# Kernel optimization log

Measured on AMD Instinct MI355X. Metric: run time of the kernel, lower is better.

Reference implementation:

```python
import jax, jax.numpy as jnp
import numpy as np

T, B, S = 8, 64, 32
DS, DT, F, H, L = 3136, 3136, 512, 512, 18
TAU = 2.0      # braincog default tau for LIFNode and all ThreeCompNode compartments
TH_MC = 1.0    # ThreeCompNode threshold
TH_LIF = 0.5   # LIFNode threshold


def setup_inputs() -> dict:
    key = jax.random.key(0)
    ks = jax.random.split(key, 6)
    return {
        "state_embedding": jax.random.normal(ks[0], (T, B, DS), jnp.float32),
        "tau_embedding": jax.random.normal(ks[1], (T, B * S, DT), jnp.float32),
        "Wb": jax.random.normal(ks[2], (F, DS), jnp.float32) * 0.02,  # basal_w (no bias)
        "Wa": jax.random.normal(ks[3], (F, DT), jnp.float32) * 0.02,  # apical_w (no bias)
        "W1": jax.random.normal(ks[4], (H, F), jnp.float32) * 0.02,
        "b1": jnp.zeros((H,), jnp.float32),
        "W2": jax.random.normal(ks[5], (L, H), jnp.float32) * 0.02,
        "b2": jnp.zeros((L,), jnp.float32),
    }


def _spike(x):
    # heaviside spike (surrogate gradient only matters for backward)
    return (x > 0).astype(x.dtype)


def reference(state_embedding, tau_embedding, Wb, Wa, W1, b1, W2, b2):
    def step(carry, inp):
        mb, ma, ms, ml = carry
        se, te = inp
        basal = (se @ Wb.T)[:, None, :]          # [B,1,F]
        apical = (te @ Wa.T).reshape(B, S, F)    # [B,S,F]
        # ThreeCompNode integral
        mb = mb + (basal - mb) / TAU
        ma = ma + (apical - ma) / TAU
        ms = ms + (ma + mb - ms) / TAU           # broadcasts to [B,S,F]
        sp = _spike(ms - TH_MC)
        ms = ms * (1.0 - jax.lax.stop_gradient(sp))  # hard reset (detached spike)
        # _last: Linear -> LIFNode -> Linear
        h = sp.reshape(B * S, F) @ W1.T + b1     # [B*S,H]
        ml = ml + (h - ml) / TAU
        sp2 = _spike(ml - TH_LIF)
        ml = ml * (1.0 - jax.lax.stop_gradient(sp2))
        out = sp2 @ W2.T + b2                    # [B*S,L]
        return (mb, ma, ms, ml), out

    init = (
        jnp.zeros((B, 1, F), jnp.float32),
        jnp.zeros((B, S, F), jnp.float32),
        jnp.zeros((B, S, F), jnp.float32),
        jnp.zeros((B * S, H), jnp.float32),
    )
    _, outs = jax.lax.scan(step, init, (state_embedding, tau_embedding))
    q = outs.mean(axis=0)                        # sum over time / time_window
    return jnp.swapaxes(q.reshape(B, S, L), 1, 2)  # [B, L, S]
```

## Files before the change

kernel.cpp:

```cpp
#include <hip/hip_runtime.h>

typedef _Float16 f16x8 __attribute__((ext_vector_type(8)));
typedef _Float16 f16x4 __attribute__((ext_vector_type(4)));
typedef float    f32x4 __attribute__((ext_vector_type(4)));

#define SPLIT_SCALE 4096.0f
#define SPLIT_INV   (1.0f / 4096.0f)

__device__ __forceinline__ void gld_lds16(const void* g, void* l) {
    __builtin_amdgcn_global_load_lds(
        (const __attribute__((address_space(1))) unsigned int*)g,
        (__attribute__((address_space(3))) unsigned int*)l,
        16, 0, 0);
}

__device__ __forceinline__ void cvt8(const float4 a, const float4 b,
                                     f16x8& h, f16x8& l) {
    float v[8] = {a.x, a.y, a.z, a.w, b.x, b.y, b.z, b.w};
#pragma unroll
    for (int j = 0; j < 8; ++j) {
        _Float16 x = (_Float16)v[j];
        h[j] = x;
        l[j] = (_Float16)((v[j] - (float)x) * SPLIT_SCALE);
    }
}

__global__ __launch_bounds__(256) void k_cvt(
    const float* __restrict__ src, _Float16* __restrict__ h, _Float16* __restrict__ l)
{
    const size_t i = ((size_t)blockIdx.x * 256 + threadIdx.x) * 8;
    float4 v0 = *(const float4*)(src + i);
    float4 v1 = *(const float4*)(src + i + 4);
    f16x8 hh, ll;
    cvt8(v0, v1, hh, ll);
    *(f16x8*)(h + i) = hh;
    *(f16x8*)(l + i) = ll;
}

__device__ __forceinline__ void front_core(
    const float* __restrict__ A,
    const _Float16* __restrict__ Bh_g, const _Float16* __restrict__ Bl_g,
    float* __restrict__ C, int K, int m0, int n0, int nIt)
{
    __shared__ _Float16 BhL[2][128 * 64];
    __shared__ _Float16 BlL[2][128 * 64];

    const int tid  = threadIdx.x;
    const int lane = tid & 63;
    const int wave = tid >> 6;
    const int quad = lane >> 4;
    const int l15  = lane & 15;

    const int srow   = wave * 32 + (lane >> 3);
    const int schunk = (((lane & 7) ^ ((lane >> 3) & 7))) * 8;
    const size_t gB  = (size_t)(n0 + srow) * (size_t)K + schunk;
    const int ldsw   = (wave * 32) * 64;

    const float* A0 = A + (size_t)(m0 + wave * 32 + l15) * (size_t)K + quad * 8;
    const float* A1 = A0 + (size_t)16 * K;

    f32x4 accm[2][8], accc[2][8];
#pragma unroll
    for (int i = 0; i < 2; ++i)
#pragma unroll
        for (int j = 0; j < 8; ++j) {
            accm[i][j] = (f32x4){0.f, 0.f, 0.f, 0.f};
            accc[i][j] = (f32x4){0.f, 0.f, 0.f, 0.f};
        }

    float4 ar[8];
    f16x8 fah[2][2], fal[2][2];

#pragma unroll
    for (int j = 0; j < 4; ++j) {
        gld_lds16(Bh_g + gB + (size_t)(8 * j) * K, BhL[0] + ldsw + 8 * j * 64);
        gld_lds16(Bl_g + gB + (size_t)(8 * j) * K, BlL[0] + ldsw + 8 * j * 64);
    }
    ar[0] = *(const float4*)(A0);      ar[1] = *(const float4*)(A0 + 4);
    ar[2] = *(const float4*)(A0 + 32); ar[3] = *(const float4*)(A0 + 36);
    ar[4] = *(const float4*)(A1);      ar[5] = *(const float4*)(A1 + 4);
    ar[6] = *(const float4*)(A1 + 32); ar[7] = *(const float4*)(A1 + 36);
#pragma unroll
    for (int i = 0; i < 2; ++i)
#pragma unroll
        for (int kc = 0; kc < 2; ++kc)
            cvt8(ar[i * 4 + kc * 2], ar[i * 4 + kc * 2 + 1], fah[i][kc], fal[i][kc]);

    for (int it = 0; it < nIt; ++it) {
        __syncthreads();
        const int cur = it & 1;
        const int nxt = cur ^ 1;
        const bool more = (it + 1) < nIt;

        if (more) {
            const size_t kb = (size_t)(it + 1) * 64;
#pragma unroll
            for (int j = 0; j < 4; ++j) {
                gld_lds16(Bh_g + gB + (size_t)(8 * j) * K + kb, BhL[nxt] + ldsw + 8 * j * 64);
                gld_lds16(Bl_g + gB + (size_t)(8 * j) * K + kb, BlL[nxt] + ldsw + 8 * j * 64);
            }
            const float* p0 = A0 + kb;
            const float* p1 = A1 + kb;
            ar[0] = *(const float4*)(p0);      ar[1] = *(const float4*)(p0 + 4);
            ar[2] = *(const float4*)(p0 + 32); ar[3] = *(const float4*)(p0 + 36);
            ar[4] = *(const float4*)(p1);      ar[5] = *(const float4*)(p1 + 4);
            ar[6] = *(const float4*)(p1 + 32); ar[7] = *(const float4*)(p1 + 36);
        }

#pragma unroll
        for (int kc = 0; kc < 2; ++kc) {
#pragma unroll
            for (int jh = 0; jh < 2; ++jh) {
                f16x8 fbh[4], fbl[4];
#pragma unroll
                for (int j = 0; j < 4; ++j) {
                    const int jj = jh * 4 + j;
                    const int p  = (((kc * 4 + quad) ^ (l15 & 7))) * 8;
                    const int e  = (jj * 16 + l15) * 64 + p;
                    fbh[j] = *(const f16x8*)&BhL[cur][e];
                    fbl[j] = *(const f16x8*)&BlL[cur][e];
                }
#pragma unroll
                for (int i = 0; i < 2; ++i)
#pragma unroll
                    for (int j = 0; j < 4; ++j) {
                        const int jj = jh * 4 + j;
                        accm[i][jj] = __builtin_amdgcn_mfma_f32_16x16x32_f16(fah[i][kc], fbh[j], accm[i][jj], 0, 0, 0);
                        accc[i][jj] = __builtin_amdgcn_mfma_f32_16x16x32_f16(fah[i][kc], fbl[j], accc[i][jj], 0, 0, 0);
                        accc[i][jj] = __builtin_amdgcn_mfma_f32_16x16x32_f16(fal[i][kc], fbh[j], accc[i][jj], 0, 0, 0);
                    }
            }
        }

        if (more) {
#pragma unroll
            for (int i = 0; i < 2; ++i)
#pragma unroll
                for (int kc = 0; kc < 2; ++kc)
                    cvt8(ar[i * 4 + kc * 2], ar[i * 4 + kc * 2 + 1], fah[i][kc], fal[i][kc]);
        }
    }

#pragma unroll
    for (int i = 0; i < 2; ++i)
#pragma unroll
        for (int jj = 0; jj < 8; ++jj)
#pragma unroll
            for (int r = 0; r < 4; ++r) {
                const int row = m0 + wave * 32 + i * 16 + quad * 4 + r;
                const int col = n0 + jj * 16 + l15;
                C[(size_t)row * 512 + col] = accm[i][jj][r] + accc[i][jj][r] * SPLIT_INV;
            }
}

__global__ __launch_bounds__(256, 2) void k_front(
    const float* __restrict__ TE, const float* __restrict__ SE,
    const _Float16* __restrict__ Wah, const _Float16* __restrict__ Wal,
    const _Float16* __restrict__ Wbh, const _Float16* __restrict__ Wbl,
    float* __restrict__ Abuf, float* __restrict__ PCb)
{
    const int bid = blockIdx.x;
    front_core(TE, Wah, Wal, Abuf, 3136, (bid & 127) * 128, (bid >> 7) * 128, 49);

    if (bid < 256) {
        __syncthreads();
        const int p   = bid >> 4;
        const int it0 = 3 * p;
        const int nIt = (p == 15) ? 4 : 3;
        const int m0  = (bid & 3) * 128;
        const int n0  = ((bid >> 2) & 3) * 128;
        front_core(SE + it0 * 64, Wbh + it0 * 64, Wbl + it0 * 64,
                   PCb + (size_t)p * 262144, 3136, m0, n0, nIt);
    }
}

__global__ __launch_bounds__(256) void k_comb(
    const float* __restrict__ PCb, float* __restrict__ Cb)
{
    const int i = (blockIdx.x * 256 + threadIdx.x) * 4;
    double s0 = 0.0, s1 = 0.0, s2 = 0.0, s3 = 0.0;
#pragma unroll
    for (int p = 0; p < 16; ++p) {
        float4 v = *(const float4*)(PCb + (size_t)p * 262144 + i);
        s0 += v.x; s1 += v.y; s2 += v.z; s3 += v.w;
    }
    *(float4*)(Cb + i) = make_float4((float)s0, (float)s1, (float)s2, (float)s3);
}

__global__ __launch_bounds__(256, 2) void k_gemm3(
    const _Float16* __restrict__ SPh, const _Float16* __restrict__ W1h,
    const _Float16* __restrict__ W1l, float* __restrict__ H)
{
    __shared__ _Float16 BhL[2][128 * 64];
    __shared__ _Float16 BlL[2][128 * 64];

    const int bid = blockIdx.x;
    const int m0 = (bid & 127) * 128, n0 = (bid >> 7) * 128;
    const int tid  = threadIdx.x;
    const int lane = tid & 63;
    const int wave = tid >> 6;
    const int quad = lane >> 4;
    const int l15  = lane & 15;

    const int srow   = wave * 32 + (lane >> 3);
    const int schunk = (((lane & 7) ^ ((lane >> 3) & 7))) * 8;
    const size_t gB  = (size_t)(n0 + srow) * 512 + schunk;
    const int ldsw   = (wave * 32) * 64;

    const _Float16* A0 = SPh + (size_t)(m0 + wave * 32 + l15) * 512 + quad * 8;
    const _Float16* A1 = A0 + (size_t)16 * 512;

    f32x4 accm[2][8], accl[2][8];
#pragma unroll
    for (int i = 0; i < 2; ++i)
#pragma unroll
        for (int j = 0; j < 8; ++j) {
            accm[i][j] = (f32x4){0.f, 0.f, 0.f, 0.f};
            accl[i][j] = (f32x4){0.f, 0.f, 0.f, 0.f};
        }

#pragma unroll
    for (int j = 0; j < 4; ++j) {
        gld_lds16(W1h + gB + (size_t)(8 * j) * 512, BhL[0] + ldsw + 8 * j * 64);
        gld_lds16(W1l + gB + (size_t)(8 * j) * 512, BlL[0] + ldsw + 8 * j * 64);
    }

    for (int it = 0; it < 8; ++it) {
        __syncthreads();
        const int cur = it & 1;
        const int nxt = cur ^ 1;
        if (it + 1 < 8) {
            const size_t kb = (size_t)(it + 1) * 64;
#pragma unroll
            for (int j = 0; j < 4; ++j) {
                gld_lds16(W1h + gB + (size_t)(8 * j) * 512 + kb, BhL[nxt] + ldsw + 8 * j * 64);
                gld_lds16(W1l + gB + (size_t)(8 * j) * 512 + kb, BlL[nxt] + ldsw + 8 * j * 64);
            }
        }
        f16x8 fa[2][2];
        const size_t ka = (size_t)it * 64;
#pragma unroll
        for (int i = 0; i < 2; ++i)
#pragma unroll
            for (int kc = 0; kc < 2; ++kc)
                fa[i][kc] = *(const f16x8*)((i ? A1 : A0) + ka + kc * 32);

#pragma unroll
        for (int kc = 0; kc < 2; ++kc) {
#pragma unroll
            for (int jh = 0; jh < 2; ++jh) {
                f16x8 fbh[4], fbl[4];
#pragma unroll
                for (int j = 0; j < 4; ++j) {
                    const int jj = jh * 4 + j;
                    const int p  = (((kc * 4 + quad) ^ (l15 & 7))) * 8;
                    const int e  = (jj * 16 + l15) * 64 + p;
                    fbh[j] = *(const f16x8*)&BhL[cur][e];
                    fbl[j] = *(const f16x8*)&BlL[cur][e];
                }
#pragma unroll
                for (int i = 0; i < 2; ++i)
#pragma unroll
                    for (int j = 0; j < 4; ++j) {
                        const int jj = jh * 4 + j;
                        accm[i][jj] = __builtin_amdgcn_mfma_f32_16x16x32_f16(fa[i][kc], fbh[j], accm[i][jj], 0, 0, 0);
                        accl[i][jj] = __builtin_amdgcn_mfma_f32_16x16x32_f16(fa[i][kc], fbl[j], accl[i][jj], 0, 0, 0);
                    }
            }
        }
    }

#pragma unroll
    for (int i = 0; i < 2; ++i)
#pragma unroll
        for (int jj = 0; jj < 8; ++jj)
#pragma unroll
            for (int r = 0; r < 4; ++r) {
                const int row = m0 + wave * 32 + i * 16 + quad * 4 + r;
                const int col = n0 + jj * 16 + l15;
                H[(size_t)row * 512 + col] = accm[i][jj][r] + accl[i][jj][r] * SPLIT_INV;
            }
}

__global__ __launch_bounds__(256) void k_scan1(
    const float* __restrict__ Abuf, const float* __restrict__ Cb,
    _Float16* __restrict__ SPh)
{
    const int idx = blockIdx.x * 256 + threadIdx.x;
    const int r = idx >> 7;
    const int f = (idx & 127) << 2;
    const int b = r >> 5;

    float mb[4] = {0, 0, 0, 0}, ma[4] = {0, 0, 0, 0}, ms[4] = {0, 0, 0, 0};
#pragma unroll
    for (int t = 0; t < 8; ++t) {
        float4 av = *(const float4*)(Abuf + ((size_t)(t * 2048 + r) << 9) + f);
        float4 bv = *(const float4*)(Cb + ((size_t)(t * 64 + b) << 9) + f);
        float a[4] = {av.x, av.y, av.z, av.w};
        float ba[4] = {bv.x, bv.y, bv.z, bv.w};
        f16x4 sp;
#pragma unroll
        for (int c = 0; c < 4; ++c) {
            mb[c] = mb[c] + (ba[c] - mb[c]) * 0.5f;
            ma[c] = ma[c] + (a[c] - ma[c]) * 0.5f;
            ms[c] = ms[c] + (ma[c] + mb[c] - ms[c]) * 0.5f;
            sp[c] = (ms[c] > 1.0f) ? (_Float16)1.0f : (_Float16)0.0f;
            ms[c] = (ms[c] > 1.0f) ? 0.0f : ms[c];
        }
        *(f16x4*)(SPh + ((size_t)(t * 2048 + r) << 9) + f) = sp;
    }
}

__global__ __launch_bounds__(256) void k_scan2(
    const float* __restrict__ H, const float* __restrict__ b1,
    float* __restrict__ spmean)
{
    const int idx = blockIdx.x * 256 + threadIdx.x;
    const int r = idx >> 7;
    const int f = (idx & 127) << 2;

    float4 b1v = *(const float4*)(b1 + f);
    float bb[4] = {b1v.x, b1v.y, b1v.z, b1v.w};
    float ml[4] = {0, 0, 0, 0}, acc[4] = {0, 0, 0, 0};
#pragma unroll
    for (int t = 0; t < 8; ++t) {
        float4 hv = *(const float4*)(H + ((size_t)(t * 2048 + r) << 9) + f);
        float h[4] = {hv.x, hv.y, hv.z, hv.w};
#pragma unroll
        for (int c = 0; c < 4; ++c) {
            float hb = h[c] + bb[c];
            ml[c] = ml[c] + (hb - ml[c]) * 0.5f;
            float s2 = (ml[c] > 0.5f) ? 1.0f : 0.0f;
            acc[c] += s2;
            ml[c] = (ml[c] > 0.5f) ? 0.0f : ml[c];
        }
    }
    *(float4*)(spmean + ((size_t)r << 9) + f) =
        make_float4(acc[0] * 0.125f, acc[1] * 0.125f, acc[2] * 0.125f, acc[3] * 0.125f);
}

__global__ __launch_bounds__(64) void k_out(
    const float* __restrict__ spmean, const float* __restrict__ W2,
    const float* __restrict__ b2, float* __restrict__ out)
{
    __shared__ float row[512];
    const int r = blockIdx.x;
    const int tid = threadIdx.x;

    const float4* src = (const float4*)(spmean + ((size_t)r << 9));
    ((float4*)row)[tid]      = src[tid];
    ((float4*)row)[tid + 64] = src[tid + 64];
    __syncthreads();

    if (tid < 18) {
        const float4* w = (const float4*)(W2 + (size_t)tid * 512);
        float acc = 0.0f;
#pragma unroll 4
        for (int c = 0; c < 128; ++c) {
            float4 wv = w[c];
            float4 rv = ((const float4*)row)[c];
            acc += rv.x * wv.x + rv.y * wv.y + rv.z * wv.z + rv.w * wv.w;
        }
        acc += b2[tid];
        const int b = r >> 5, s = r & 31;
        out[((size_t)(b * 18 + tid) << 5) + s] = acc;
    }
}

extern "C" void kernel_launch(void* const* d_in, const int* in_sizes, int n_in,
                              void* d_out, int out_size, void* d_ws, size_t ws_size,
                              hipStream_t stream)
{
    const float* SE = (const float*)d_in[0];
    const float* TE = (const float*)d_in[1];
    const float* Wb = (const float*)d_in[2];
    const float* Wa = (const float*)d_in[3];
    const float* W1 = (const float*)d_in[4];
    const float* b1 = (const float*)d_in[5];
    const float* W2 = (const float*)d_in[6];
    const float* b2 = (const float*)d_in[7];
    float* out = (float*)d_out;

    char* ws = (char*)d_ws;
    size_t off = 0;
    float*    Abuf   = (float*)(ws + off);     off += 33554432;
    float*    Cb     = (float*)(ws + off);     off += 1048576;
    float*    spmean = (float*)(ws + off);     off += 4194304;
    _Float16* SPh    = (_Float16*)(ws + off);  off += 16777216;
    _Float16* W1h    = (_Float16*)(ws + off);  off += 524288;
    _Float16* W1l    = (_Float16*)(ws + off);  off += 524288;
    _Float16* Wah    = (_Float16*)(ws + off);  off += 3211264;
    _Float16* Wal    = (_Float16*)(ws + off);  off += 3211264;
    _Float16* Wbh    = (_Float16*)(ws + off);  off += 3211264;
    _Float16* Wbl    = (_Float16*)(ws + off);  off += 3211264;

    float* PCb = (float*)SPh;

    hipLaunchKernelGGL(k_cvt, dim3(784), dim3(256), 0, stream, Wa, Wah, Wal);
    hipLaunchKernelGGL(k_cvt, dim3(784), dim3(256), 0, stream, Wb, Wbh, Wbl);
    hipLaunchKernelGGL(k_cvt, dim3(128), dim3(256), 0, stream, W1, W1h, W1l);

    hipLaunchKernelGGL(k_front, dim3(512), dim3(256), 0, stream,
                       TE, SE, Wah, Wal, Wbh, Wbl, Abuf, PCb);
    hipLaunchKernelGGL(k_comb, dim3(256), dim3(256), 0, stream, PCb, Cb);
    hipLaunchKernelGGL(k_scan1, dim3(1024), dim3(256), 0, stream, Abuf, Cb, SPh);
    hipLaunchKernelGGL(k_gemm3, dim3(512), dim3(256), 0, stream, SPh, W1h, W1l, Abuf);
    hipLaunchKernelGGL(k_scan2, dim3(1024), dim3(256), 0, stream, Abuf, b1, spmean);
    hipLaunchKernelGGL(k_out, dim3(2048), dim3(64), 0, stream, spmean, W2, b2, out);
}
```

Before: 502.7 us.

## Merge weight conversions, widen scan1 per thread, fuse scan2 with output GEMV

The three weight-conversion launches become one kernel that picks its source by block index. The first scan now processes eight features per thread with paired float4 loads and 16-byte spike stores, using half as many blocks. The second LIF scan is fused with the final W2 projection: spike means stay in shared memory, and each wave reduces a dot product with shuffles. This removes the spmean round trip through global memory and two launches. The cost is that each block rereads W2, though it should stay cached.

Result: faster. 486.2 us (median of 2 runs) (-3.3%).

```diff
diff --git a/kernel.cpp b/kernel.cpp
--- a/kernel.cpp
+++ b/kernel.cpp
@@ -25,10 +25,21 @@
     }
 }
 
-__global__ __launch_bounds__(256) void k_cvt(
-    const float* __restrict__ src, _Float16* __restrict__ h, _Float16* __restrict__ l)
-{
-    const size_t i = ((size_t)blockIdx.x * 256 + threadIdx.x) * 8;
+__global__ __launch_bounds__(256) void k_cvt_all(
+    const float* __restrict__ Wa, const float* __restrict__ Wb,
+    const float* __restrict__ W1,
+    _Float16* __restrict__ Wah, _Float16* __restrict__ Wal,
+    _Float16* __restrict__ Wbh, _Float16* __restrict__ Wbl,
+    _Float16* __restrict__ W1h, _Float16* __restrict__ W1l)
+{
+    int b = blockIdx.x;
+    const float* src;
+    _Float16 *h, *l;
+    if (b < 784)        { src = Wa; h = Wah; l = Wal; }
+    else if (b < 1568)  { src = Wb; h = Wbh; l = Wbl; b -= 784; }
+    else                { src = W1; h = W1h; l = W1l; b -= 1568; }
+
+    const size_t i = ((size_t)b * 256 + threadIdx.x) * 8;
     float4 v0 = *(const float4*)(src + i);
     float4 v1 = *(const float4*)(src + i + 4);
     f16x8 hh, ll;
@@ -287,37 +298,44 @@
     _Float16* __restrict__ SPh)
 {
     const int idx = blockIdx.x * 256 + threadIdx.x;
-    const int r = idx >> 7;
-    const int f = (idx & 127) << 2;
+    const int r = idx >> 6;
+    const int f = (idx & 63) << 3;
     const int b = r >> 5;
 
-    float mb[4] = {0, 0, 0, 0}, ma[4] = {0, 0, 0, 0}, ms[4] = {0, 0, 0, 0};
+    float mb[8] = {0}, ma[8] = {0}, ms[8] = {0};
 #pragma unroll
     for (int t = 0; t < 8; ++t) {
-        float4 av = *(const float4*)(Abuf + ((size_t)(t * 2048 + r) << 9) + f);
-        float4 bv = *(const float4*)(Cb + ((size_t)(t * 64 + b) << 9) + f);
-        float a[4] = {av.x, av.y, av.z, av.w};
-        float ba[4] = {bv.x, bv.y, bv.z, bv.w};
-        f16x4 sp;
-#pragma unroll
-        for (int c = 0; c < 4; ++c) {
+        const size_t ra = ((size_t)(t * 2048 + r) << 9) + f;
+        const size_t rb = ((size_t)(t * 64 + b) << 9) + f;
+        float4 av0 = *(const float4*)(Abuf + ra);
+        float4 av1 = *(const float4*)(Abuf + ra + 4);
+        float4 bv0 = *(const float4*)(Cb + rb);
+        float4 bv1 = *(const float4*)(Cb + rb + 4);
+        float a[8]  = {av0.x, av0.y, av0.z, av0.w, av1.x, av1.y, av1.z, av1.w};
+        float ba[8] = {bv0.x, bv0.y, bv0.z, bv0.w, bv1.x, bv1.y, bv1.z, bv1.w};
+        f16x8 sp;
+#pragma unroll
+        for (int c = 0; c < 8; ++c) {
             mb[c] = mb[c] + (ba[c] - mb[c]) * 0.5f;
             ma[c] = ma[c] + (a[c] - ma[c]) * 0.5f;
             ms[c] = ms[c] + (ma[c] + mb[c] - ms[c]) * 0.5f;
             sp[c] = (ms[c] > 1.0f) ? (_Float16)1.0f : (_Float16)0.0f;
             ms[c] = (ms[c] > 1.0f) ? 0.0f : ms[c];
         }
-        *(f16x4*)(SPh + ((size_t)(t * 2048 + r) << 9) + f) = sp;
-    }
-}
-
-__global__ __launch_bounds__(256) void k_scan2(
+        *(f16x8*)(SPh + ra) = sp;
+    }
+}
+
+__global__ __launch_bounds__(256) void k_tail(
     const float* __restrict__ H, const float* __restrict__ b1,
-    float* __restrict__ spmean)
-{
-    const int idx = blockIdx.x * 256 + threadIdx.x;
-    const int r = idx >> 7;
-    const int f = (idx & 127) << 2;
+    const float* __restrict__ W2, const float* __restrict__ b2,
+    float* __restrict__ out)
+{
+    __shared__ float sm[2][512];
+    const int tid  = threadIdx.x;
+    const int half = tid >> 7;
+    const int r    = blockIdx.x * 2 + half;
+    const int f    = (tid & 127) << 2;
 
     float4 b1v = *(const float4*)(b1 + f);
     float bb[4] = {b1v.x, b1v.y, b1v.z, b1v.w};
@@ -335,35 +353,29 @@
             ml[c] = (ml[c] > 0.5f) ? 0.0f : ml[c];
         }
     }
-    *(float4*)(spmean + ((size_t)r << 9) + f) =
+    *(float4*)&sm[half][f] =
         make_float4(acc[0] * 0.125f, acc[1] * 0.125f, acc[2] * 0.125f, acc[3] * 0.125f);
-}
-
-__global__ __launch_bounds__(64) void k_out(
-    const float* __restrict__ spmean, const float* __restrict__ W2,
-    const float* __restrict__ b2, float* __restrict__ out)
-{
-    __shared__ float row[512];
-    const int r = blockIdx.x;
-    const int tid = threadIdx.x;
-
-    const float4* src = (const float4*)(spmean + ((size_t)r << 9));
-    ((float4*)row)[tid]      = src[tid];
-    ((float4*)row)[tid + 64] = src[tid + 64];
     __syncthreads();
 
-    if (tid < 18) {
-        const float4* w = (const float4*)(W2 + (size_t)tid * 512);
-        float acc = 0.0f;
-#pragma unroll 4
-        for (int c = 0; c < 128; ++c) {
-            float4 wv = w[c];
-            float4 rv = ((const float4*)row)[c];
-            acc += rv.x * wv.x + rv.y * wv.y + rv.z * wv.z + rv.w * wv.w;
-        }
-        acc += b2[tid];
-        const int b = r >> 5, s = r & 31;
-        out[((size_t)(b * 18 + tid) << 5) + s] = acc;
+    const int wave = tid >> 6;
+    const int lane = tid & 63;
+#pragma unroll
+    for (int d = wave; d < 36; d += 4) {
+        const int row = (d >= 18) ? 1 : 0;
+        const int l   = d - row * 18;
+        const float4 w0 = *(const float4*)(W2 + (size_t)l * 512 + lane * 8);
+        const float4 w1 = *(const float4*)(W2 + (size_t)l * 512 + lane * 8 + 4);
+        const float4 s0 = *(const float4*)&sm[row][lane * 8];
+        const float4 s1 = *(const float4*)&sm[row][lane * 8 + 4];
+        float p = s0.x * w0.x + s0.y * w0.y + s0.z * w0.z + s0.w * w0.w
+                + s1.x * w1.x + s1.y * w1.y + s1.z * w1.z + s1.w * w1.w;
+#pragma unroll
+        for (int off = 32; off; off >>= 1) p += __shfl_xor(p, off);
+        if (lane == 0) {
+            const int rr = blockIdx.x * 2 + row;
+            const int b = rr >> 5, s = rr & 31;
+            out[((size_t)(b * 18 + l) << 5) + s] = p + b2[l];
+        }
     }
 }
 
@@ -385,7 +397,7 @@
     size_t off = 0;
     float*    Abuf   = (float*)(ws + off);     off += 33554432;
     float*    Cb     = (float*)(ws + off);     off += 1048576;
-    float*    spmean = (float*)(ws + off);     off += 4194304;
+    float*    spare  = (float*)(ws + off);     off += 4194304;
     _Float16* SPh    = (_Float16*)(ws + off);  off += 16777216;
     _Float16* W1h    = (_Float16*)(ws + off);  off += 524288;
     _Float16* W1l    = (_Float16*)(ws + off);  off += 524288;
@@ -393,18 +405,16 @@
     _Float16* Wal    = (_Float16*)(ws + off);  off += 3211264;
     _Float16* Wbh    = (_Float16*)(ws + off);  off += 3211264;
     _Float16* Wbl    = (_Float16*)(ws + off);  off += 3211264;
+    (void)spare;
 
     float* PCb = (float*)SPh;
 
-    hipLaunchKernelGGL(k_cvt, dim3(784), dim3(256), 0, stream, Wa, Wah, Wal);
-    hipLaunchKernelGGL(k_cvt, dim3(784), dim3(256), 0, stream, Wb, Wbh, Wbl);
-    hipLaunchKernelGGL(k_cvt, dim3(128), dim3(256), 0, stream, W1, W1h, W1l);
-
+    hipLaunchKernelGGL(k_cvt_all, dim3(1696), dim3(256), 0, stream,
+                       Wa, Wb, W1, Wah, Wal, Wbh, Wbl, W1h, W1l);
     hipLaunchKernelGGL(k_front, dim3(512), dim3(256), 0, stream,
                        TE, SE, Wah, Wal, Wbh, Wbl, Abuf, PCb);
     hipLaunchKernelGGL(k_comb, dim3(256), dim3(256), 0, stream, PCb, Cb);
-    hipLaunchKernelGGL(k_scan1, dim3(1024), dim3(256), 0, stream, Abuf, Cb, SPh);
+    hipLaunchKernelGGL(k_scan1, dim3(512), dim3(256), 0, stream, Abuf, Cb, SPh);
     hipLaunchKernelGGL(k_gemm3, dim3(512), dim3(256), 0, stream, SPh, W1h, W1l, Abuf);
-    hipLaunchKernelGGL(k_scan2, dim3(1024), dim3(256), 0, stream, Abuf, b1, spmean);
-    hipLaunchKernelGGL(k_out, dim3(2048), dim3(64), 0, stream, spmean, W2, b2, out);
-}
+    hipLaunchKernelGGL(k_tail, dim3(1024), dim3(256), 0, stream, Abuf, b1, W2, b2, out);
+}
```
